# Performance work log

Measured on AMD Instinct MI355X. Metric: run time of the kernel, lower is better.

## Reference

```python
import jax, jax.numpy as jnp
import numpy as np

D_MODEL = 2048
H_Q = 32
H_KV = 8
D_HEAD = D_MODEL // H_Q   # 64
G = H_Q // H_KV           # 4 query heads per kv head
B, S = 2, 2048


def setup_inputs() -> dict:
    key = jax.random.key(0)
    ks = jax.random.split(key, 7)
    s = 0.02  # weight init scale
    return {
        "q": jax.random.normal(ks[0], (B, S, D_MODEL), jnp.float32),
        "k": jax.random.normal(ks[1], (B, S, D_MODEL), jnp.float32),
        "v": jax.random.normal(ks[2], (B, S, D_MODEL), jnp.float32),
        "Wq": jax.random.normal(ks[3], (D_MODEL, D_MODEL), jnp.float32) * s,
        "Wk": jax.random.normal(ks[4], (D_MODEL, H_KV * D_HEAD), jnp.float32) * s,
        "Wv": jax.random.normal(ks[5], (D_MODEL, H_KV * D_HEAD), jnp.float32) * s,
        "Wo": jax.random.normal(ks[6], (D_MODEL, D_MODEL), jnp.float32) * s,
    }


def reference(q, k, v, Wq, Wk, Wv, Wo):
    # Projections (torch Linear with bias=False: x @ W^T; here W stored as [in,out])
    b, s, _ = q.shape
    # repeat_interleave(k, G, -2) maps kv head j -> query heads j*G..j*G+G-1,
    # i.e. query head h uses kv head h // G. Reshape q heads as (H_KV, G)
    # kv-head-major instead of materializing expanded K/V.
    qh = (q @ Wq).reshape(b, s, H_KV, G, D_HEAD)
    kh = (k @ Wk).reshape(b, s, H_KV, D_HEAD)
    vh = (v @ Wv).reshape(b, s, H_KV, D_HEAD)
    scale = 1.0 / jnp.sqrt(jnp.asarray(D_HEAD, qh.dtype))
    # scores: [B, H_KV, G, Sq, Sk]
    scores = jnp.einsum('bqhgd,bkhd->bhgqk', qh, kh) * scale
    attn = jax.nn.softmax(scores, axis=-1)
    # context: [B, Sq, H_KV, G, D_HEAD]
    ctx = jnp.einsum('bhgqk,bkhd->bqhgd', attn, vh)
    out = ctx.reshape(b, s, D_MODEL) @ Wo
    return out
```

## Files before the change

kernel.cpp:

```cpp
#include <hip/hip_runtime.h>
#include <stdint.h>


typedef __attribute__((ext_vector_type(8))) short short8;
typedef __attribute__((ext_vector_type(4))) float float4v;
typedef __attribute__((ext_vector_type(4))) unsigned short ushort4v;
typedef __attribute__((ext_vector_type(4))) unsigned int uint4v;

__device__ __forceinline__ unsigned short f2bf(float f) {
  union { float f; unsigned int u; } v; v.f = f;
  unsigned int r = v.u + 0x7fffu + ((v.u >> 16) & 1u);
  return (unsigned short)(r >> 16);
}
__device__ __forceinline__ unsigned int fbits(float f) {
  union { float f; unsigned int u; } v; v.f = f; return v.u;
}
__device__ __forceinline__ unsigned int pack_bf16_trunc(float lo, float hi) {
  return __builtin_amdgcn_perm(fbits(hi), fbits(lo), 0x07060302u);
}

__device__ __forceinline__ void gl2lds16(const unsigned short* g, unsigned short* l) {
  __builtin_amdgcn_global_load_lds(
      (const __attribute__((address_space(1))) void*)g,
      (__attribute__((address_space(3))) void*)l, 16, 0, 0);
}

__global__ void prep(const float* __restrict__ q, const float* __restrict__ k,
                     const float* __restrict__ v,
                     const float* __restrict__ Wq, const float* __restrict__ Wk,
                     const float* __restrict__ Wv,
                     unsigned short* __restrict__ qb, unsigned short* __restrict__ kb,
                     unsigned short* __restrict__ vb,
                     unsigned short* __restrict__ WTq, unsigned short* __restrict__ WTk,
                     unsigned short* __restrict__ WTv)
{
  __shared__ unsigned short t[32][33];
  const int z = blockIdx.z;
  if (z >= 3) {
    const float* in  = (z == 3) ? q : (z == 4) ? k : v;
    unsigned short* out = (z == 3) ? qb : (z == 4) ? kb : vb;
    const int tid = threadIdx.y * 32 + threadIdx.x;
    const int bid = blockIdx.y * 64 + blockIdx.x;
    for (int i = bid * 256 + tid; i < 2097152; i += 4096 * 256) {
      const float4v a = *(const float4v*)(in + (size_t)i * 4);
      *(ushort4v*)(out + (size_t)i * 4) = (ushort4v){f2bf(a.x), f2bf(a.y), f2bf(a.z), f2bf(a.w)};
    }
    return;
  }
  const float* in; unsigned short* out; int R, C;
  if (z == 0)      { in = Wq; out = WTq; R = 2048; C = 2048; }
  else if (z == 1) { in = Wk; out = WTk; R = 2048; C = 512; }
  else             { in = Wv; out = WTv; R = 2048; C = 512; }
  const int x0 = blockIdx.x * 32, y0 = blockIdx.y * 32;
  if (x0 >= C) return;
  const int tx = threadIdx.x, ty = threadIdx.y;
#pragma unroll
  for (int i = 0; i < 4; ++i) {
    const int r = y0 + ty + i * 8, c = x0 + tx;
    t[ty + i * 8][tx] = f2bf(in[(size_t)r * C + c]);
  }
  __syncthreads();
#pragma unroll
  for (int i = 0; i < 4; ++i)
    out[(size_t)(x0 + ty + i * 8) * R + y0 + tx] = t[tx][ty + i * 8];
}

__global__ void transpose_bf16(const float* __restrict__ inp, unsigned short* __restrict__ out,
                               int R, int C) {
  __shared__ unsigned short t[32][33];
  const int x0 = blockIdx.x * 32, y0 = blockIdx.y * 32;
  const int tx = threadIdx.x, ty = threadIdx.y;
#pragma unroll
  for (int i = 0; i < 4; ++i) {
    const int r = y0 + ty + i * 8, c = x0 + tx;
    t[ty + i * 8][tx] = f2bf(inp[(size_t)r * C + c]);
  }
  __syncthreads();
#pragma unroll
  for (int i = 0; i < 4; ++i)
    out[(size_t)(x0 + ty + i * 8) * R + y0 + tx] = t[tx][ty + i * 8];
}

template<int TN, bool C_BF16>
__device__ void gemm_body(const unsigned short* __restrict__ A,
                          const unsigned short* __restrict__ Bt,
                          void* __restrict__ C, int N, int K, float cscale,
                          int bx, int by)
{
  constexpr int NT = TN / 32;
  constexpr int BI = TN / 64;
  __shared__ unsigned short As[128][32];
  __shared__ unsigned short Bs[TN][32];

  const int tid  = threadIdx.x;
  const int wave = tid >> 6;
  const int lane = tid & 63;
  const int quad = lane >> 4;
  const int l15  = lane & 15;
  const int wm   = (wave >> 1) * 64;
  const int wn   = (wave & 1) * (TN / 2);
  const int m0   = by * 128;
  const int n0   = bx * TN;

  const int srow = lane >> 2;
  const int skof = (lane & 3) * 8;

  float4v acc[4][NT];
#pragma unroll
  for (int i = 0; i < 4; ++i)
#pragma unroll
    for (int j = 0; j < NT; ++j) acc[i][j] = (float4v)0.0f;

  for (int k0 = 0; k0 < K; k0 += 32) {
    __syncthreads();
#pragma unroll
    for (int i = 0; i < 2; ++i) {
      const int row = wave * 32 + i * 16 + srow;
      gl2lds16(A + (size_t)(m0 + row) * K + k0 + skof, &As[wave * 32 + i * 16][0]);
    }
#pragma unroll
    for (int i = 0; i < BI; ++i) {
      const int row = wave * (TN / 4) + i * 16 + srow;
      gl2lds16(Bt + (size_t)(n0 + row) * K + k0 + skof, &Bs[wave * (TN / 4) + i * 16][0]);
    }
    __syncthreads();

    short8 af[4], bf[NT];
#pragma unroll
    for (int mt = 0; mt < 4; ++mt)  af[mt] = *(const short8*)&As[wm + mt * 16 + l15][quad * 8];
#pragma unroll
    for (int nt = 0; nt < NT; ++nt) bf[nt] = *(const short8*)&Bs[wn + nt * 16 + l15][quad * 8];
#pragma unroll
    for (int mt = 0; mt < 4; ++mt)
#pragma unroll
      for (int nt = 0; nt < NT; ++nt)
        acc[mt][nt] = __builtin_amdgcn_mfma_f32_16x16x32_bf16(af[mt], bf[nt], acc[mt][nt], 0, 0, 0);
  }

#pragma unroll
  for (int mt = 0; mt < 4; ++mt)
#pragma unroll
    for (int nt = 0; nt < NT; ++nt) {
      const int row = m0 + wm + mt * 16 + quad * 4;
      const int col = n0 + wn + nt * 16 + l15;
#pragma unroll
      for (int r = 0; r < 4; ++r) {
        const float val = acc[mt][nt][r] * cscale;
        if (C_BF16) ((unsigned short*)C)[(size_t)(row + r) * N + col] = f2bf(val);
        else        ((float*)C)[(size_t)(row + r) * N + col] = val;
      }
    }
}

template<int TN, bool C_BF16>
__global__ __launch_bounds__(256, 2)
void gemm_bt(const unsigned short* __restrict__ A, const unsigned short* __restrict__ Bt,
             void* __restrict__ C, int N, int K, float cscale)
{
  gemm_body<TN, C_BF16>(A, Bt, C, N, K, cscale, blockIdx.x, blockIdx.y);
}

__global__ __launch_bounds__(256, 2)
void gemm_kv(const unsigned short* __restrict__ kb, const unsigned short* __restrict__ WTk,
             unsigned short* __restrict__ Kp,
             const unsigned short* __restrict__ WTv, const unsigned short* __restrict__ vb,
             unsigned short* __restrict__ VpT)
{
  const int id = blockIdx.x;
  if (id < 256) gemm_body<64, true>(kb, WTk, Kp, 512, 2048, 1.0f, id & 7, id >> 3);
  else          gemm_body<64, true>(WTv, vb, VpT, 4096, 2048, 1.0f, (id - 256) & 63, (id - 256) >> 6);
}

__global__ __launch_bounds__(256, 4)
void attn_flash(const unsigned short* __restrict__ Qp,
                const unsigned short* __restrict__ Kp,
                const unsigned short* __restrict__ VpT,
                unsigned short* __restrict__ Ctx)
{
  __shared__ unsigned short Ks[2][64 * 64];
  __shared__ unsigned short VTs[2][64 * 64];

  const int tid  = threadIdx.x;
  const int wave = tid >> 6;
  const int lane = tid & 63;
  const int quad = lane >> 4;
  const int l15  = lane & 15;

  const int head = blockIdx.y;
  const int b    = head >> 5;
  const int hq   = head & 31;
  const int hkv  = hq >> 2;
  const size_t qrow = (size_t)(b * 2048 + blockIdx.x * 128 + wave * 32);

  short8 qf[2][2];
#pragma unroll
  for (int mt = 0; mt < 2; ++mt)
#pragma unroll
    for (int kc = 0; kc < 2; ++kc)
      qf[mt][kc] = *(const short8*)&Qp[(qrow + mt * 16 + l15) * 2048 + hq * 64 + kc * 32 + quad * 8];

  float4v oa[2][4];
  float4v lacc[2];
#pragma unroll
  for (int mt = 0; mt < 2; ++mt) {
    lacc[mt] = (float4v)0.0f;
#pragma unroll
    for (int dt = 0; dt < 4; ++dt) oa[mt][dt] = (float4v)0.0f;
  }
  short8 ones;
#pragma unroll
  for (int i = 0; i < 8; ++i) ones[i] = (short)0x3F80;

  auto stage = [&](int j, int bu) {
#pragma unroll
    for (int i = 0; i < 2; ++i) {
      const int s  = i * 256 + wave * 64 + lane;
      const int r  = s >> 3;
      const int lc = (s & 7) ^ (r & 7);
      const int rk = ((r >> 4) & 1) * 32 + ((r >> 2) & 3) * 8 + (r >> 5) * 4 + (r & 3);
      gl2lds16(Kp + (size_t)(b * 2048 + j * 64 + rk) * 512 + hkv * 64 + lc * 8,
               &Ks[bu][i * 2048 + wave * 512]);
      gl2lds16(VpT + (size_t)(hkv * 64 + r) * 4096 + b * 2048 + j * 64 + lc * 8,
               &VTs[bu][i * 2048 + wave * 512]);
    }
  };

  stage(0, 0);
  __syncthreads();

  for (int j = 0; j < 32; ++j) {
    const int bu = j & 1;
    if (j < 31) stage(j + 1, bu ^ 1);

    short8 kf[4][2];
#pragma unroll
    for (int nt = 0; nt < 4; ++nt) {
      const int krow = nt * 16 + l15;
      kf[nt][0] = *(const short8*)&Ks[bu][krow * 64 + ((quad ^ (l15 & 7)) * 8)];
      kf[nt][1] = *(const short8*)&Ks[bu][krow * 64 + (((4 + quad) ^ (l15 & 7)) * 8)];
    }

    __builtin_amdgcn_s_setprio(1);

    unsigned int w[2][4][2];
#pragma unroll
    for (int mt = 0; mt < 2; ++mt) {
#pragma unroll
      for (int nt = 0; nt < 4; ++nt) {
        float4v sa = (float4v)0.0f;
        sa = __builtin_amdgcn_mfma_f32_16x16x32_bf16(kf[nt][0], qf[mt][0], sa, 0, 0, 0);
        sa = __builtin_amdgcn_mfma_f32_16x16x32_bf16(kf[nt][1], qf[mt][1], sa, 0, 0, 0);
        const float e0 = __builtin_amdgcn_exp2f(sa[0]);
        const float e1 = __builtin_amdgcn_exp2f(sa[1]);
        const float e2 = __builtin_amdgcn_exp2f(sa[2]);
        const float e3 = __builtin_amdgcn_exp2f(sa[3]);
        w[mt][nt][0] = pack_bf16_trunc(e0, e1);
        w[mt][nt][1] = pack_bf16_trunc(e2, e3);
      }
    }

#pragma unroll
    for (int kc = 0; kc < 2; ++kc) {
      union { uint4v u; short8 s; } p0u, p1u;
      p0u.u = (uint4v){w[0][kc][0], w[0][kc][1], w[0][kc + 2][0], w[0][kc + 2][1]};
      p1u.u = (uint4v){w[1][kc][0], w[1][kc][1], w[1][kc + 2][0], w[1][kc + 2][1]};
      const short8 pf0 = p0u.s;
      const short8 pf1 = p1u.s;
#pragma unroll
      for (int dt = 0; dt < 4; ++dt) {
        const int vrow = dt * 16 + l15;
        const short8 vf = *(const short8*)&VTs[bu][vrow * 64 + (((kc * 4 + quad) ^ (l15 & 7)) * 8)];
        oa[0][dt] = __builtin_amdgcn_mfma_f32_16x16x32_bf16(pf0, vf, oa[0][dt], 0, 0, 0);
        oa[1][dt] = __builtin_amdgcn_mfma_f32_16x16x32_bf16(pf1, vf, oa[1][dt], 0, 0, 0);
      }
      lacc[0] = __builtin_amdgcn_mfma_f32_16x16x32_bf16(pf0, ones, lacc[0], 0, 0, 0);
      lacc[1] = __builtin_amdgcn_mfma_f32_16x16x32_bf16(pf1, ones, lacc[1], 0, 0, 0);
    }

    __builtin_amdgcn_s_setprio(0);
    __syncthreads();
  }

#pragma unroll
  for (int mt = 0; mt < 2; ++mt)
#pragma unroll
    for (int r = 0; r < 4; ++r) {
      const float inv = 1.0f / lacc[mt][r];
#pragma unroll
      for (int dt = 0; dt < 4; ++dt)
        Ctx[(qrow + mt * 16 + quad * 4 + r) * 2048 + hq * 64 + dt * 16 + l15] =
            f2bf(oa[mt][dt][r] * inv);
    }
}

extern "C" void kernel_launch(void* const* d_in, const int* in_sizes, int n_in,
                              void* d_out, int out_size, void* d_ws, size_t ws_size,
                              hipStream_t stream)
{
  const float* q  = (const float*)d_in[0];
  const float* k  = (const float*)d_in[1];
  const float* v  = (const float*)d_in[2];
  const float* Wq = (const float*)d_in[3];
  const float* Wk = (const float*)d_in[4];
  const float* Wv = (const float*)d_in[5];
  const float* Wo = (const float*)d_in[6];
  float* out = (float*)d_out;

  unsigned short* ws  = (unsigned short*)d_ws;
  unsigned short* qb  = ws;
  unsigned short* kb  = qb  + (size_t)8388608;
  unsigned short* vb  = kb  + (size_t)8388608;
  unsigned short* WT  = vb  + (size_t)8388608;
  unsigned short* Qp  = WT  + (size_t)4194304;
  unsigned short* Kp  = Qp  + (size_t)8388608;
  unsigned short* VpT = Kp  + (size_t)2097152;
  unsigned short* Ctx = qb;
  unsigned short* WTk = Qp;
  unsigned short* WTv = Qp + (size_t)1048576;

  const dim3 blk(256);
  const dim3 tblk(32, 8);
  const float SM_SCALE = 0.125f * 1.44269504089f;

  prep<<<dim3(64, 64, 6), tblk, 0, stream>>>(q, k, v, Wq, Wk, Wv,
                                             qb, kb, vb, WT, WTk, WTv);

  gemm_kv<<<dim3(512), blk, 0, stream>>>(kb, WTk, Kp, WTv, vb, VpT);

  gemm_bt<128, true><<<dim3(16, 32), blk, 0, stream>>>(qb, WT, Qp, 2048, 2048, SM_SCALE);

  transpose_bf16<<<dim3(64, 64), tblk, 0, stream>>>(Wo, WT, 2048, 2048);

  attn_flash<<<dim3(16, 64), blk, 0, stream>>>(Qp, Kp, VpT, Ctx);

  gemm_bt<128, false><<<dim3(16, 32), blk, 0, stream>>>(Ctx, WT, out, 2048, 2048, 1.0f);
}
```

Measured before the change: 382.7 us.

## Merge Q/K/V projections into one launch and fold Wo transpose into attention

Combines the K/V projection GEMM and the Q projection GEMM into a single 768-block launch using 128-wide tiles, so the small K/V work fills the machine alongside Q. The Wo transpose kernel is removed and its work is done by 64 extra blocks appended to the attention grid, overlapping with attention. Block indices are swizzled across groups of 8 (likely to spread neighbouring tiles across XCDs) for better L2 locality. WTk/WTv are staged in the output buffer so WT remains free, and this depends on the output being overwritten later.

```diff
diff --git a/kernel.cpp b/kernel.cpp
--- a/kernel.cpp
+++ b/kernel.cpp
@@ -65,22 +65,6 @@
     out[(size_t)(x0 + ty + i * 8) * R + y0 + tx] = t[tx][ty + i * 8];
 }
 
-__global__ void transpose_bf16(const float* __restrict__ inp, unsigned short* __restrict__ out,
-                               int R, int C) {
-  __shared__ unsigned short t[32][33];
-  const int x0 = blockIdx.x * 32, y0 = blockIdx.y * 32;
-  const int tx = threadIdx.x, ty = threadIdx.y;
-#pragma unroll
-  for (int i = 0; i < 4; ++i) {
-    const int r = y0 + ty + i * 8, c = x0 + tx;
-    t[ty + i * 8][tx] = f2bf(inp[(size_t)r * C + c]);
-  }
-  __syncthreads();
-#pragma unroll
-  for (int i = 0; i < 4; ++i)
-    out[(size_t)(x0 + ty + i * 8) * R + y0 + tx] = t[tx][ty + i * 8];
-}
-
 template<int TN, bool C_BF16>
 __device__ void gemm_body(const unsigned short* __restrict__ A,
                           const unsigned short* __restrict__ Bt,
@@ -152,35 +136,71 @@
     }
 }
 
-template<int TN, bool C_BF16>
 __global__ __launch_bounds__(256, 2)
-void gemm_bt(const unsigned short* __restrict__ A, const unsigned short* __restrict__ Bt,
-             void* __restrict__ C, int N, int K, float cscale)
-{
-  gemm_body<TN, C_BF16>(A, Bt, C, N, K, cscale, blockIdx.x, blockIdx.y);
-}
-
+void gemm_mid(const unsigned short* __restrict__ qb, const unsigned short* __restrict__ WTq,
+              unsigned short* __restrict__ Qp,
+              const unsigned short* __restrict__ kb, const unsigned short* __restrict__ WTk,
+              unsigned short* __restrict__ Kp,
+              const unsigned short* __restrict__ WTv, const unsigned short* __restrict__ vb,
+              unsigned short* __restrict__ VpT, float sm_scale)
+{
+  const int id = blockIdx.x;
+  if (id < 512) {
+    const int s = (id & 7) * 64 + (id >> 3);
+    gemm_body<128, true>(qb, WTq, Qp, 2048, 2048, sm_scale, s & 15, s >> 4);
+  } else if (id < 640) {
+    const int t = id - 512;
+    const int s = (t & 7) * 16 + (t >> 3);
+    gemm_body<128, true>(kb, WTk, Kp, 512, 2048, 1.0f, s & 3, s >> 2);
+  } else {
+    const int t = id - 640;
+    const int s = (t & 7) * 16 + (t >> 3);
+    gemm_body<128, true>(WTv, vb, VpT, 4096, 2048, 1.0f, s & 31, s >> 5);
+  }
+}
+
+template<int TN, bool C_BF16, int GX>
 __global__ __launch_bounds__(256, 2)
-void gemm_kv(const unsigned short* __restrict__ kb, const unsigned short* __restrict__ WTk,
-             unsigned short* __restrict__ Kp,
-             const unsigned short* __restrict__ WTv, const unsigned short* __restrict__ vb,
-             unsigned short* __restrict__ VpT)
-{
-  const int id = blockIdx.x;
-  if (id < 256) gemm_body<64, true>(kb, WTk, Kp, 512, 2048, 1.0f, id & 7, id >> 3);
-  else          gemm_body<64, true>(WTv, vb, VpT, 4096, 2048, 1.0f, (id - 256) & 63, (id - 256) >> 6);
+void gemm_swz(const unsigned short* __restrict__ A, const unsigned short* __restrict__ Bt,
+              void* __restrict__ C, int N, int K, float cscale)
+{
+  const int chunk = gridDim.x >> 3;
+  const int s = (blockIdx.x & 7) * chunk + (blockIdx.x >> 3);
+  gemm_body<TN, C_BF16>(A, Bt, C, N, K, cscale, s % GX, s / GX);
 }
 
 __global__ __launch_bounds__(256, 4)
 void attn_flash(const unsigned short* __restrict__ Qp,
                 const unsigned short* __restrict__ Kp,
                 const unsigned short* __restrict__ VpT,
-                unsigned short* __restrict__ Ctx)
+                unsigned short* __restrict__ Ctx,
+                const float* __restrict__ Wo,
+                unsigned short* __restrict__ WTo)
 {
   __shared__ unsigned short Ks[2][64 * 64];
   __shared__ unsigned short VTs[2][64 * 64];
 
   const int tid  = threadIdx.x;
+
+  if (blockIdx.y >= 64) {
+    unsigned short (*t)[33] = (unsigned short (*)[33])&Ks[0][0];
+    const int bid = (blockIdx.y - 64) * 16 + blockIdx.x;
+    const int tx = tid & 31, ty = tid >> 5;
+    for (int tt = 0; tt < 64; ++tt) {
+      const int tile = bid * 64 + tt;
+      const int x0 = (tile & 63) * 32, y0 = (tile >> 6) * 32;
+#pragma unroll
+      for (int i = 0; i < 4; ++i)
+        t[ty + i * 8][tx] = f2bf(Wo[(size_t)(y0 + ty + i * 8) * 2048 + x0 + tx]);
+      __syncthreads();
+#pragma unroll
+      for (int i = 0; i < 4; ++i)
+        WTo[(size_t)(x0 + ty + i * 8) * 2048 + y0 + tx] = t[tx][ty + i * 8];
+      __syncthreads();
+    }
+    return;
+  }
+
   const int wave = tid >> 6;
   const int lane = tid & 63;
   const int quad = lane >> 4;
@@ -315,8 +335,8 @@
   unsigned short* Kp  = Qp  + (size_t)8388608;
   unsigned short* VpT = Kp  + (size_t)2097152;
   unsigned short* Ctx = qb;
-  unsigned short* WTk = Qp;
-  unsigned short* WTv = Qp + (size_t)1048576;
+  unsigned short* WTk = (unsigned short*)d_out;
+  unsigned short* WTv = (unsigned short*)d_out + 1048576;
 
   const dim3 blk(256);
   const dim3 tblk(32, 8);
@@ -325,13 +345,9 @@
   prep<<<dim3(64, 64, 6), tblk, 0, stream>>>(q, k, v, Wq, Wk, Wv,
                                              qb, kb, vb, WT, WTk, WTv);
 
-  gemm_kv<<<dim3(512), blk, 0, stream>>>(kb, WTk, Kp, WTv, vb, VpT);
-
-  gemm_bt<128, true><<<dim3(16, 32), blk, 0, stream>>>(qb, WT, Qp, 2048, 2048, SM_SCALE);
-
-  transpose_bf16<<<dim3(64, 64), tblk, 0, stream>>>(Wo, WT, 2048, 2048);
-
-  attn_flash<<<dim3(16, 64), blk, 0, stream>>>(Qp, Kp, VpT, Ctx);
-
-  gemm_bt<128, false><<<dim3(16, 32), blk, 0, stream>>>(Ctx, WT, out, 2048, 2048, 1.0f);
-}
+  gemm_mid<<<dim3(768), blk, 0, stream>>>(qb, WT, Qp, kb, WTk, Kp, WTv, vb, VpT, SM_SCALE);
+
+  attn_flash<<<dim3(16, 68), blk, 0, stream>>>(Qp, Kp, VpT, Ctx, Wo, WT);
+
+  gemm_swz<128, false, 16><<<dim3(512), blk, 0, stream>>>(Ctx, WT, out, 2048, 2048, 1.0f);
+}
```

Result: slower. 397.4 us (+3.9%).
